# Kernel tuning notes

Measured on AMD Instinct MI355X. Metric: run time of the kernel, lower is better.

Reference implementation:

```python
import jax, jax.numpy as jnp
import numpy as np


def setup_inputs() -> dict:
    key = jax.random.key(0)
    k1, k2, k3 = jax.random.split(key, 3)
    b, n, d, K = 8, 16384, 128, 128
    X = jax.random.normal(k1, (b, n, d), dtype=jnp.float32)
    C = jax.random.normal(k2, (K, d), dtype=jnp.float32)
    # module init: scale.data.uniform_(-1, 0)
    S = -jax.random.uniform(k3, (K,), dtype=jnp.float32)
    return {"X": X, "C": C, "S": S}


def reference(X, C, S):
    """Soft VQ encoding: scaled L2 -> softmax assignment -> residual aggregation.

    X: (b, n, d) features; C: (k, d) codewords; S: (k,) scales.
    Returns E: (b, k, d) aggregated residuals, same math as
    aggregate(softmax(scaled_l2(X, C, S), dim=2), X, C).
    """
    X2 = jnp.sum(X * X, axis=-1, keepdims=True)          # (b, n, 1)
    C2 = jnp.sum(C * C, axis=-1)                          # (k,)
    XC = jnp.einsum('bnd,kd->bnk', X, C)                  # (b, n, k)
    D = S * (X2 + C2 - 2.0 * XC)                          # scaled L2, (b, n, k)
    A = jax.nn.softmax(D, axis=-1)                        # assignment weights
    # E[b,k,:] = sum_n A[b,n,k] * (X[b,n,:] - C[k,:])
    #          = (A^T X)[b,k,:] - (sum_n A[b,n,k]) * C[k,:]
    E = jnp.einsum('bnk,bnd->bkd', A, X) - jnp.sum(A, axis=1)[..., None] * C[None]
    return E
```

## Files before the change

kernel.cpp:

```cpp
#include <hip/hip_runtime.h>


#define NN   16384
#define ND   128
#define NK   128
#define NC   64
#define TT   2
#define BPB  128
#define CBP  136
#define XTP  72
#define ATP  72

typedef __bf16 bf16x8 __attribute__((ext_vector_type(8)));
typedef float  f32x4  __attribute__((ext_vector_type(4)));

__device__ __forceinline__ unsigned short f2bf(float x) {
    unsigned int u = __float_as_uint(x);
    u = (u + 0x7fffu + ((u >> 16) & 1u)) >> 16;
    return (unsigned short)u;
}
__device__ __forceinline__ float bf2f(unsigned short u) {
    return __uint_as_float(((unsigned int)u) << 16);
}

__global__ __launch_bounds__(256, 2) void vq_main(
    const float* __restrict__ Xg, const float* __restrict__ Cg,
    const float* __restrict__ Sg, unsigned short* __restrict__ Pg)
{
    __shared__ __align__(16) unsigned short sCb[NK * CBP];
    __shared__ __align__(16) unsigned short sXT[ND * XTP];
    __shared__ __align__(16) unsigned short sAt[NK * ATP];
    __shared__ __align__(16) float2 sST[NK];
    __shared__ __align__(16) float  sC2[NK];

    const int tid  = threadIdx.x;
    const int lane = tid & 63;
    const int wave = tid >> 6;
    const int l15  = lane & 15;
    const int quad = lane >> 4;
    const int bid  = blockIdx.x;
    const int b    = bid >> 7;
    const int bg   = bid & (BPB - 1);

    #pragma unroll
    for (int it = 0; it < 16; ++it) {
        int flat = it * 256 + tid;
        int row  = flat >> 5;
        int c4   = flat & 31;
        float4 v = reinterpret_cast<const float4*>(Cg)[row * 32 + c4];
        ushort4 h;
        h.x = f2bf(v.x); h.y = f2bf(v.y); h.z = f2bf(v.z); h.w = f2bf(v.w);
        *reinterpret_cast<ushort4*>(&sCb[row * CBP + c4 * 4]) = h;
        float ss = v.x*v.x + v.y*v.y + v.z*v.z + v.w*v.w;
        ss += __shfl_xor(ss, 1);
        ss += __shfl_xor(ss, 2);
        ss += __shfl_xor(ss, 4);
        ss += __shfl_xor(ss, 8);
        ss += __shfl_xor(ss, 16);
        if ((lane & 31) == 0) sC2[row] = ss;
    }
    __syncthreads();
    if (tid < NK) {
        float s = Sg[tid];
        sST[tid] = make_float2(s, s * sC2[tid]);
    }

    f32x4 eacc[2][8];
    #pragma unroll
    for (int i = 0; i < 2; ++i)
        #pragma unroll
        for (int j = 0; j < 8; ++j)
            eacc[i][j] = (f32x4){0.f, 0.f, 0.f, 0.f};
    f32x4 cntacc[2];
    cntacc[0] = (f32x4){0.f, 0.f, 0.f, 0.f};
    cntacc[1] = (f32x4){0.f, 0.f, 0.f, 0.f};

    union CU { unsigned short u[8]; bf16x8 v; };
    CU one8;
    #pragma unroll
    for (int j = 0; j < 8; ++j) one8.u[j] = 0x3F80;

    const float* Xb = Xg + (size_t)b * (NN * ND);
    const int rloc = wave * 16 + l15;

    #pragma unroll 1
    for (int t = 0; t < TT; ++t) {
        const int chunk = bg * TT + t;
        const float* rp = Xb + (size_t)(chunk * NC + rloc) * ND;

        CU cu[4];
        float x2 = 0.f;
        #pragma unroll
        for (int ks = 0; ks < 4; ++ks) {
            float4 va = *reinterpret_cast<const float4*>(rp + ks * 32 + quad * 8);
            float4 vb = *reinterpret_cast<const float4*>(rp + ks * 32 + quad * 8 + 4);
            x2 += va.x*va.x + va.y*va.y + va.z*va.z + va.w*va.w;
            x2 += vb.x*vb.x + vb.y*vb.y + vb.z*vb.z + vb.w*vb.w;
            cu[ks].u[0] = f2bf(va.x); cu[ks].u[1] = f2bf(va.y);
            cu[ks].u[2] = f2bf(va.z); cu[ks].u[3] = f2bf(va.w);
            cu[ks].u[4] = f2bf(vb.x); cu[ks].u[5] = f2bf(vb.y);
            cu[ks].u[6] = f2bf(vb.z); cu[ks].u[7] = f2bf(vb.w);
        }
        x2 += __shfl_xor(x2, 16);
        x2 += __shfl_xor(x2, 32);

        __syncthreads();

        #pragma unroll
        for (int ks = 0; ks < 4; ++ks) {
            #pragma unroll
            for (int j = 0; j < 8; ++j) {
                int d  = ks * 32 + quad * 8 + j;
                int rs = rloc ^ (((d >> 3) & 3) << 3);
                sXT[d * XTP + rs] = cu[ks].u[j];
            }
        }

        f32x4 dacc[8];
        #pragma unroll
        for (int mt = 0; mt < 8; ++mt) {
            f32x4 acc = (f32x4){0.f, 0.f, 0.f, 0.f};
            #pragma unroll
            for (int ks = 0; ks < 4; ++ks) {
                bf16x8 af = *reinterpret_cast<const bf16x8*>(
                    &sCb[(mt * 16 + l15) * CBP + ks * 32 + quad * 8]);
                acc = __builtin_amdgcn_mfma_f32_16x16x32_bf16(af, cu[ks].v, acc, 0, 0, 0);
            }
            dacc[mt] = acc;
        }

        float mx = -3.0e38f;
        #pragma unroll
        for (int mt = 0; mt < 8; ++mt) {
            #pragma unroll
            for (int r = 0; r < 4; ++r) {
                float2 st = sST[mt * 16 + quad * 4 + r];
                float dv = st.x * fmaf(-2.f, dacc[mt][r], x2) + st.y;
                dacc[mt][r] = dv;
                mx = fmaxf(mx, dv);
            }
        }
        mx = fmaxf(mx, __shfl_xor(mx, 16));
        mx = fmaxf(mx, __shfl_xor(mx, 32));
        float ls = 0.f;
        #pragma unroll
        for (int mt = 0; mt < 8; ++mt) {
            #pragma unroll
            for (int r = 0; r < 4; ++r) {
                float e = __expf(dacc[mt][r] - mx);
                dacc[mt][r] = e;
                ls += e;
            }
        }
        ls += __shfl_xor(ls, 16);
        ls += __shfl_xor(ls, 32);
        const float inv = 1.0f / ls;

        #pragma unroll
        for (int mt = 0; mt < 8; ++mt) {
            #pragma unroll
            for (int r = 0; r < 4; ++r) {
                float a = dacc[mt][r] * inv;
                sAt[(mt * 16 + quad * 4 + r) * ATP + rloc] = f2bf(a);
            }
        }

        __syncthreads();

        #pragma unroll
        for (int mt2 = 0; mt2 < 2; ++mt2) {
            const int cwrow = wave * 32 + mt2 * 16 + l15;
            bf16x8 a0 = *reinterpret_cast<const bf16x8*>(&sAt[cwrow * ATP + quad * 8]);
            bf16x8 a1 = *reinterpret_cast<const bf16x8*>(&sAt[cwrow * ATP + 32 + quad * 8]);
            cntacc[mt2] = __builtin_amdgcn_mfma_f32_16x16x32_bf16(a0, one8.v, cntacc[mt2], 0, 0, 0);
            cntacc[mt2] = __builtin_amdgcn_mfma_f32_16x16x32_bf16(a1, one8.v, cntacc[mt2], 0, 0, 0);
            #pragma unroll
            for (int dt = 0; dt < 8; ++dt) {
                const int drow = dt * 16 + l15;
                const int sw = ((drow >> 3) & 3) << 3;
                const unsigned short* xp = &sXT[drow * XTP];
                bf16x8 b0 = *reinterpret_cast<const bf16x8*>(&xp[(quad * 8) ^ sw]);
                bf16x8 b1 = *reinterpret_cast<const bf16x8*>(&xp[(32 + quad * 8) ^ sw]);
                eacc[mt2][dt] = __builtin_amdgcn_mfma_f32_16x16x32_bf16(a0, b0, eacc[mt2][dt], 0, 0, 0);
                eacc[mt2][dt] = __builtin_amdgcn_mfma_f32_16x16x32_bf16(a1, b1, eacc[mt2][dt], 0, 0, 0);
            }
        }
    }

    unsigned short* P = Pg + (size_t)bid * (NK * ND);
    #pragma unroll
    for (int mt2 = 0; mt2 < 2; ++mt2) {
        #pragma unroll
        for (int r = 0; r < 4; ++r) {
            const int cw = wave * 32 + mt2 * 16 + quad * 4 + r;
            const float cc = cntacc[mt2][r];
            const float* crow = Cg + cw * ND;
            #pragma unroll
            for (int dt = 0; dt < 8; ++dt) {
                const int d = dt * 16 + l15;
                P[cw * ND + d] = f2bf(eacc[mt2][dt][r] - cc * crow[d]);
            }
        }
    }
}

__global__ __launch_bounds__(256) void vq_reduce(
    const unsigned short* __restrict__ Pg, float* __restrict__ Eg)
{
    const int g  = blockIdx.x * 256 + threadIdx.x;
    const int b  = g >> 12;
    const int i4 = g & 4095;
    const unsigned short* base = Pg + (size_t)(b * BPB) * (NK * ND) + i4 * 4;
    float a0 = 0.f, a1 = 0.f, a2 = 0.f, a3 = 0.f;
    #pragma unroll 8
    for (int j = 0; j < BPB; ++j) {
        ushort4 v = *reinterpret_cast<const ushort4*>(base + (size_t)j * (NK * ND));
        a0 += bf2f(v.x); a1 += bf2f(v.y); a2 += bf2f(v.z); a3 += bf2f(v.w);
    }
    float4 o; o.x = a0; o.y = a1; o.z = a2; o.w = a3;
    *reinterpret_cast<float4*>(Eg + (size_t)b * (NK * ND) + i4 * 4) = o;
}

extern "C" void kernel_launch(void* const* d_in, const int* in_sizes, int n_in,
                              void* d_out, int out_size, void* d_ws, size_t ws_size,
                              hipStream_t stream) {
    const float* X = (const float*)d_in[0];
    const float* C = (const float*)d_in[1];
    const float* S = (const float*)d_in[2];
    float* E = (float*)d_out;
    (void)n_in; (void)in_sizes; (void)out_size; (void)ws_size;

    unsigned short* P = (unsigned short*)d_ws;

    hipLaunchKernelGGL(vq_main,   dim3(1024), dim3(256), 0, stream, X, C, S, P);
    hipLaunchKernelGGL(vq_reduce, dim3(128),  dim3(256), 0, stream, P, E);
}
```

Measured before the change: 136.9 us.

## Prefetch next X chunk, halve block count, use native bf16 casts

Each block now handles four chunks instead of two, so the grid shrinks to 512 blocks and the partial buffer that vq_reduce sums is half as large. The first half of the next chunk's X row is loaded into registers before the current chunk's MFMA and softmax work, hiding part of the global load latency. Manual bf16 rounding is replaced with native __bf16 casts, which may map to hardware conversion instructions, and the scale table is read with float4 vector loads. The trade-offs are higher register pressure and fewer blocks per CU to hide latency.

```diff
diff --git a/kernel.cpp b/kernel.cpp
--- a/kernel.cpp
+++ b/kernel.cpp
@@ -5,8 +5,8 @@
 #define ND   128
 #define NK   128
 #define NC   64
-#define TT   2
-#define BPB  128
+#define TT   4
+#define BPB  64
 #define CBP  136
 #define XTP  72
 #define ATP  72
@@ -14,11 +14,9 @@
 typedef __bf16 bf16x8 __attribute__((ext_vector_type(8)));
 typedef float  f32x4  __attribute__((ext_vector_type(4)));
 
-__device__ __forceinline__ unsigned short f2bf(float x) {
-    unsigned int u = __float_as_uint(x);
-    u = (u + 0x7fffu + ((u >> 16) & 1u)) >> 16;
-    return (unsigned short)u;
-}
+union CU  { __bf16 b[8]; unsigned short u[8]; bf16x8 v; };
+union HH4 { __bf16 b[4]; ushort4 s; };
+
 __device__ __forceinline__ float bf2f(unsigned short u) {
     return __uint_as_float(((unsigned int)u) << 16);
 }
@@ -39,7 +37,7 @@
     const int l15  = lane & 15;
     const int quad = lane >> 4;
     const int bid  = blockIdx.x;
-    const int b    = bid >> 7;
+    const int b    = bid >> 6;
     const int bg   = bid & (BPB - 1);
 
     #pragma unroll
@@ -48,9 +46,10 @@
         int row  = flat >> 5;
         int c4   = flat & 31;
         float4 v = reinterpret_cast<const float4*>(Cg)[row * 32 + c4];
-        ushort4 h;
-        h.x = f2bf(v.x); h.y = f2bf(v.y); h.z = f2bf(v.z); h.w = f2bf(v.w);
-        *reinterpret_cast<ushort4*>(&sCb[row * CBP + c4 * 4]) = h;
+        HH4 h;
+        h.b[0] = (__bf16)v.x; h.b[1] = (__bf16)v.y;
+        h.b[2] = (__bf16)v.z; h.b[3] = (__bf16)v.w;
+        *reinterpret_cast<ushort4*>(&sCb[row * CBP + c4 * 4]) = h.s;
         float ss = v.x*v.x + v.y*v.y + v.z*v.z + v.w*v.w;
         ss += __shfl_xor(ss, 1);
         ss += __shfl_xor(ss, 2);
@@ -75,36 +74,70 @@
     cntacc[0] = (f32x4){0.f, 0.f, 0.f, 0.f};
     cntacc[1] = (f32x4){0.f, 0.f, 0.f, 0.f};
 
-    union CU { unsigned short u[8]; bf16x8 v; };
     CU one8;
     #pragma unroll
     for (int j = 0; j < 8; ++j) one8.u[j] = 0x3F80;
 
     const float* Xb = Xg + (size_t)b * (NN * ND);
     const int rloc = wave * 16 + l15;
+
+    float4 raw[4];
+    {
+        const float* rp0 = Xb + (size_t)(bg * TT * NC + rloc) * ND;
+        raw[0] = *reinterpret_cast<const float4*>(rp0 + quad * 8);
+        raw[1] = *reinterpret_cast<const float4*>(rp0 + quad * 8 + 4);
+        raw[2] = *reinterpret_cast<const float4*>(rp0 + 32 + quad * 8);
+        raw[3] = *reinterpret_cast<const float4*>(rp0 + 32 + quad * 8 + 4);
+    }
 
     #pragma unroll 1
     for (int t = 0; t < TT; ++t) {
         const int chunk = bg * TT + t;
         const float* rp = Xb + (size_t)(chunk * NC + rloc) * ND;
 
+        float4 va2 = *reinterpret_cast<const float4*>(rp + 64 + quad * 8);
+        float4 vb2 = *reinterpret_cast<const float4*>(rp + 64 + quad * 8 + 4);
+        float4 va3 = *reinterpret_cast<const float4*>(rp + 96 + quad * 8);
+        float4 vb3 = *reinterpret_cast<const float4*>(rp + 96 + quad * 8 + 4);
+
         CU cu[4];
         float x2 = 0.f;
         #pragma unroll
-        for (int ks = 0; ks < 4; ++ks) {
-            float4 va = *reinterpret_cast<const float4*>(rp + ks * 32 + quad * 8);
-            float4 vb = *reinterpret_cast<const float4*>(rp + ks * 32 + quad * 8 + 4);
+        for (int ks = 0; ks < 2; ++ks) {
+            float4 va = raw[ks * 2], vb = raw[ks * 2 + 1];
             x2 += va.x*va.x + va.y*va.y + va.z*va.z + va.w*va.w;
             x2 += vb.x*vb.x + vb.y*vb.y + vb.z*vb.z + vb.w*vb.w;
-            cu[ks].u[0] = f2bf(va.x); cu[ks].u[1] = f2bf(va.y);
-            cu[ks].u[2] = f2bf(va.z); cu[ks].u[3] = f2bf(va.w);
-            cu[ks].u[4] = f2bf(vb.x); cu[ks].u[5] = f2bf(vb.y);
-            cu[ks].u[6] = f2bf(vb.z); cu[ks].u[7] = f2bf(vb.w);
+            cu[ks].b[0] = (__bf16)va.x; cu[ks].b[1] = (__bf16)va.y;
+            cu[ks].b[2] = (__bf16)va.z; cu[ks].b[3] = (__bf16)va.w;
+            cu[ks].b[4] = (__bf16)vb.x; cu[ks].b[5] = (__bf16)vb.y;
+            cu[ks].b[6] = (__bf16)vb.z; cu[ks].b[7] = (__bf16)vb.w;
+        }
+        {
+            x2 += va2.x*va2.x + va2.y*va2.y + va2.z*va2.z + va2.w*va2.w;
+            x2 += vb2.x*vb2.x + vb2.y*vb2.y + vb2.z*vb2.z + vb2.w*vb2.w;
+            cu[2].b[0] = (__bf16)va2.x; cu[2].b[1] = (__bf16)va2.y;
+            cu[2].b[2] = (__bf16)va2.z; cu[2].b[3] = (__bf16)va2.w;
+            cu[2].b[4] = (__bf16)vb2.x; cu[2].b[5] = (__bf16)vb2.y;
+            cu[2].b[6] = (__bf16)vb2.z; cu[2].b[7] = (__bf16)vb2.w;
+            x2 += va3.x*va3.x + va3.y*va3.y + va3.z*va3.z + va3.w*va3.w;
+            x2 += vb3.x*vb3.x + vb3.y*vb3.y + vb3.z*vb3.z + vb3.w*vb3.w;
+            cu[3].b[0] = (__bf16)va3.x; cu[3].b[1] = (__bf16)va3.y;
+            cu[3].b[2] = (__bf16)va3.z; cu[3].b[3] = (__bf16)va3.w;
+            cu[3].b[4] = (__bf16)vb3.x; cu[3].b[5] = (__bf16)vb3.y;
+            cu[3].b[6] = (__bf16)vb3.z; cu[3].b[7] = (__bf16)vb3.w;
         }
         x2 += __shfl_xor(x2, 16);
         x2 += __shfl_xor(x2, 32);
 
         __syncthreads();
+
+        if (t + 1 < TT) {
+            const float* rpn = rp + (size_t)NC * ND;
+            raw[0] = *reinterpret_cast<const float4*>(rpn + quad * 8);
+            raw[1] = *reinterpret_cast<const float4*>(rpn + quad * 8 + 4);
+            raw[2] = *reinterpret_cast<const float4*>(rpn + 32 + quad * 8);
+            raw[3] = *reinterpret_cast<const float4*>(rpn + 32 + quad * 8 + 4);
+        }
 
         #pragma unroll
         for (int ks = 0; ks < 4; ++ks) {
@@ -132,13 +165,15 @@
         float mx = -3.0e38f;
         #pragma unroll
         for (int mt = 0; mt < 8; ++mt) {
-            #pragma unroll
-            for (int r = 0; r < 4; ++r) {
-                float2 st = sST[mt * 16 + quad * 4 + r];
-                float dv = st.x * fmaf(-2.f, dacc[mt][r], x2) + st.y;
-                dacc[mt][r] = dv;
-                mx = fmaxf(mx, dv);
-            }
+            float4 s01 = *reinterpret_cast<const float4*>(&sST[mt * 16 + quad * 4]);
+            float4 s23 = *reinterpret_cast<const float4*>(&sST[mt * 16 + quad * 4 + 2]);
+            float dv0 = s01.x * fmaf(-2.f, dacc[mt][0], x2) + s01.y;
+            float dv1 = s01.z * fmaf(-2.f, dacc[mt][1], x2) + s01.w;
+            float dv2 = s23.x * fmaf(-2.f, dacc[mt][2], x2) + s23.y;
+            float dv3 = s23.z * fmaf(-2.f, dacc[mt][3], x2) + s23.w;
+            dacc[mt][0] = dv0; dacc[mt][1] = dv1;
+            dacc[mt][2] = dv2; dacc[mt][3] = dv3;
+            mx = fmaxf(mx, fmaxf(fmaxf(dv0, dv1), fmaxf(dv2, dv3)));
         }
         mx = fmaxf(mx, __shfl_xor(mx, 16));
         mx = fmaxf(mx, __shfl_xor(mx, 32));
@@ -161,7 +196,8 @@
             #pragma unroll
             for (int r = 0; r < 4; ++r) {
                 float a = dacc[mt][r] * inv;
-                sAt[(mt * 16 + quad * 4 + r) * ATP + rloc] = f2bf(a);
+                *reinterpret_cast<__bf16*>(
+                    &sAt[(mt * 16 + quad * 4 + r) * ATP + rloc]) = (__bf16)a;
             }
         }
 
@@ -198,7 +234,8 @@
             #pragma unroll
             for (int dt = 0; dt < 8; ++dt) {
                 const int d = dt * 16 + l15;
-                P[cw * ND + d] = f2bf(eacc[mt2][dt][r] - cc * crow[d]);
+                *reinterpret_cast<__bf16*>(&P[cw * ND + d]) =
+                    (__bf16)(eacc[mt2][dt][r] - cc * crow[d]);
             }
         }
     }
@@ -232,6 +269,6 @@
 
     unsigned short* P = (unsigned short*)d_ws;
 
-    hipLaunchKernelGGL(vq_main,   dim3(1024), dim3(256), 0, stream, X, C, S, P);
-    hipLaunchKernelGGL(vq_reduce, dim3(128),  dim3(256), 0, stream, P, E);
-}
+    hipLaunchKernelGGL(vq_main,   dim3(512), dim3(256), 0, stream, X, C, S, P);
+    hipLaunchKernelGGL(vq_reduce, dim3(128), dim3(256), 0, stream, P, E);
+}
```

New measurement: 115.4 us. 1.19x faster.
